# Kernel optimization log

Measured on AMD Instinct MI355X. Metric: run time of the kernel, lower is better.

## Reference

```python
import jax, jax.numpy as jnp
import numpy as np

N = 100000      # hits
K = 256         # max truth objects per event
C = 2           # n_ccoords
NCLS = 6        # n_classes
Q_MIN = 0.5
S_B = 1.0
ENERGY_DEN_OFFSET = 1.0
PAYLOAD_BETA_CLIP = 0.1
USE_AVG_CC = 0.0
BETA_CLIP = 1.0 - 1e-5


def _divide_no_nan(num, den):
    return jnp.where(den == 0.0, 0.0, num / jnp.where(den == 0.0, 1.0, den))


def setup_inputs() -> dict:
    key = jax.random.key(0)
    ks = jax.random.split(key, 12)
    pred_beta = jax.random.uniform(ks[0], (N, 1), minval=0.01, maxval=0.99)
    pred_ccoords = jax.random.normal(ks[1], (N, C))
    pred_energy = jax.random.uniform(ks[2], (N, 1), minval=0.0, maxval=100.0)
    pred_pos = 50.0 * jax.random.normal(ks[3], (N, 2))
    pred_time = jax.random.normal(ks[4], (N, 1))
    pred_id = jax.random.normal(ks[5], (N, NCLS))
    t_energy = jax.random.uniform(ks[6], (N, 1), minval=0.1, maxval=100.0)
    t_pos = 50.0 * jax.random.normal(ks[7], (N, 2))
    t_time = jax.random.normal(ks[8], (N, 1))
    t_pid = jax.random.randint(ks[9], (N, 1), 1, NCLS + 1).astype(jnp.float32)
    t_idx = jax.random.randint(ks[10], (N, 1), -1, K)  # -1 == noise
    rowsplits = jnp.array([0, N], dtype=jnp.int32)
    return dict(pred_beta=pred_beta, pred_ccoords=pred_ccoords,
                pred_energy=pred_energy, pred_pos=pred_pos,
                pred_time=pred_time, pred_id=pred_id,
                t_energy=t_energy, t_pos=t_pos, t_time=t_time, t_pid=t_pid,
                t_idx=t_idx, rowsplits=rowsplits)


def oc_loss(pred_beta, pred_ccoords, pred_energy, pred_pos, pred_time,
            pred_id, t_energy, t_pos, t_time, t_pid, t_idx):
    beta = jnp.clip(pred_beta[:, 0], 0.0, BETA_CLIP)          # [N]
    q = jnp.arctanh(beta) ** 2 + Q_MIN                        # [N] charge
    tidx = t_idx[:, 0]
    not_noise = tidx >= 0                                     # [N]
    tclip = jnp.where(not_noise, tidx, 0)

    # hit->object assignment matrix [N, K]
    M = jax.nn.one_hot(tclip, K, dtype=beta.dtype) * not_noise[:, None].astype(beta.dtype)
    counts = M.sum(axis=0)                                    # [K]
    obj_valid = counts > 0.0
    n_valid = jnp.maximum(obj_valid.sum().astype(beta.dtype), 1.0)

    # condensation point per object: highest-beta hit of that object
    score = jnp.where(M > 0.0, beta[:, None], -1.0)           # [N, K]
    alpha = jnp.argmax(score, axis=0)                         # [K]
    x_alpha = pred_ccoords[alpha]                             # [K, C]
    mean_cc = (M.T @ pred_ccoords) / jnp.maximum(counts, 1.0)[:, None]
    x_k = USE_AVG_CC * mean_cc + (1.0 - USE_AVG_CC) * x_alpha
    q_alpha = q[alpha]                                        # [K]
    beta_alpha = beta[alpha]

    # pairwise hit <-> condensation-point squared distances [N, K]
    diff = pred_ccoords[:, None, :] - x_k[None, :, :]
    distsq = jnp.sum(diff * diff, axis=-1)

    qq = q[:, None] * q_alpha[None, :]                        # [N, K]
    # attractive potential: own-object hits pulled toward condensation point
    v_att_k = (M * distsq * qq).sum(axis=0) / jnp.maximum(counts, 1.0)
    V_att = jnp.where(obj_valid, v_att_k, 0.0).sum() / n_valid
    # repulsive potential: all other hits pushed out of a unit ball
    hinge = jax.nn.relu(1.0 - jnp.sqrt(distsq + 1e-6))
    v_rep_k = ((1.0 - M) * hinge * qq).sum(axis=0) / jnp.maximum(N - counts, 1.0)
    V_rep = jnp.where(obj_valid, v_rep_k, 0.0).sum() / n_valid

    # beta terms: sharpen condensation points, suppress noise beta
    L_beta = jnp.where(obj_valid, 1.0 - beta_alpha, 0.0).sum() / n_valid
    n_noise = jnp.maximum((~not_noise).astype(beta.dtype).sum(), 1.0)
    L_noise = S_B * jnp.where(not_noise, 0.0, beta).sum() / n_noise

    # --- per-hit payload losses ---
    ew = jax.nn.relu(jnp.where(t_energy > 10.0,
                               1.0, (t_energy - 0.5) / 10.0 * 10.0 / 9.5))
    e_loss = _divide_no_nan((t_energy - pred_energy) ** 2,
                            t_energy + ENERGY_DEN_OFFSET)
    p_loss = jnp.sum((t_pos - pred_pos) ** 2, axis=-1, keepdims=True) / 100.0
    tm_loss = (t_time - pred_time) ** 2
    cls_loss = 1e-8 * jnp.mean(pred_id ** 2, axis=-1, keepdims=True)
    payload = jnp.concatenate([e_loss, p_loss, tm_loss, cls_loss], axis=-1) * ew  # [N,4]
    payload = jnp.where(pred_beta < PAYLOAD_BETA_CLIP, 0.0, payload)

    # beta-weighted average of payload over each truth object
    pw = beta * not_noise.astype(beta.dtype)                  # [N]
    num = M.T @ (payload * pw[:, None])                       # [K, 4]
    den = (M * pw[:, None]).sum(axis=0)                       # [K]
    per_obj = num / jnp.maximum(den, 1e-6)[:, None]
    L_payload = (jnp.where(obj_valid[:, None], per_obj, 0.0).sum(axis=0) / n_valid).sum()

    return V_att + V_rep + L_beta + L_noise + L_payload


def reference(pred_beta, pred_ccoords, pred_energy, pred_pos, pred_time,
              pred_id, t_energy, t_pos, t_time, t_pid, t_idx, rowsplits):
    return oc_loss(pred_beta, pred_ccoords, pred_energy, pred_pos, pred_time,
                   pred_id, t_energy, t_pos, t_time, t_pid, t_idx)
```

## Files before the change

### kernel.cpp

```cpp
#include <hip/hip_runtime.h>
#include <math.h>

#define KOBJ 256
#define B1   256
#define NW   4
#define WSTR 257
#define QMIN 0.5f
#define BETA_CLIP_C (1.0f - 1e-5f)

typedef unsigned long long u64;

__global__ __launch_bounds__(256) void partials(
    const float*  __restrict__ pred_beta,
    const float*  __restrict__ pred_energy,
    const float2* __restrict__ pred_pos,
    const float*  __restrict__ pred_time,
    const float2* __restrict__ pred_id2,
    const float*  __restrict__ t_energy,
    const float2* __restrict__ t_pos,
    const float*  __restrict__ t_time,
    const int*    __restrict__ t_idx,
    u64*    __restrict__ pk_part,
    float*  __restrict__ cnt_part,
    float*  __restrict__ den_part,
    float*  __restrict__ num_part,
    float*  __restrict__ noise_part,
    int n)
{
    __shared__ u64   spk[NW][WSTR];
    __shared__ float scnt[NW][WSTR], sden[NW][WSTR], snum[NW][WSTR];
    __shared__ float snoise[256];
    int t = threadIdx.x;
    int b = blockIdx.x;
    int w = t >> 6;
    for (int i = t; i < NW * WSTR; i += 256) {
        ((u64*)spk)[i] = 0;
        ((float*)scnt)[i] = 0.f;
        ((float*)sden)[i] = 0.f;
        ((float*)snum)[i] = 0.f;
    }
    __syncthreads();

    float noise = 0.0f;
    for (int i = b * 256 + t; i < n; i += B1 * 256) {
        int tid = t_idx[i];
        float braw = pred_beta[i];
        float beta = fminf(fmaxf(braw, 0.0f), BETA_CLIP_C);
        if (tid >= 0) {
            atomicAdd(&scnt[w][tid], 1.0f);
            u64 key = ((u64)__float_as_uint(beta) << 32) |
                      (u64)(0x7FFFFFFFu - (unsigned)i);
            atomicMax(&spk[w][tid], key);
            float te = t_energy[i];
            float ew = (te > 10.0f) ? 1.0f : fmaxf(0.0f, (te - 0.5f) / 9.5f);
            float de = te - pred_energy[i];
            float el = de * de / (te + 1.0f);
            float2 tp = t_pos[i];
            float2 pp = pred_pos[i];
            float dpx = tp.x - pp.x, dpy = tp.y - pp.y;
            float pl = (dpx * dpx + dpy * dpy) * 0.01f;
            float dt = t_time[i] - pred_time[i];
            float tl = dt * dt;
            float2 id0 = pred_id2[3 * i];
            float2 id1 = pred_id2[3 * i + 1];
            float2 id2 = pred_id2[3 * i + 2];
            float cs = id0.x * id0.x + id0.y * id0.y + id1.x * id1.x +
                       id1.y * id1.y + id2.x * id2.x + id2.y * id2.y;
            cs *= (1e-8f / 6.0f);
            float mask = (braw < 0.1f) ? 0.0f : 1.0f;
            float wgt = mask * ew * beta;
            atomicAdd(&sden[w][tid], beta);
            atomicAdd(&snum[w][tid], (el + pl + tl + cs) * wgt);
        } else {
            noise += beta;
        }
    }
    __syncthreads();
    u64 pk = spk[0][t];
    { u64 q = spk[1][t]; if (q > pk) pk = q; }
    { u64 q = spk[2][t]; if (q > pk) pk = q; }
    { u64 q = spk[3][t]; if (q > pk) pk = q; }
    float cnt = scnt[0][t] + scnt[1][t] + scnt[2][t] + scnt[3][t];
    float den = sden[0][t] + sden[1][t] + sden[2][t] + sden[3][t];
    float num = snum[0][t] + snum[1][t] + snum[2][t] + snum[3][t];
    int o = t * B1 + b;
    pk_part[o]  = pk;
    cnt_part[o] = cnt;
    den_part[o] = den;
    num_part[o] = num;
    snoise[t] = noise;
    __syncthreads();
    for (int s = 128; s > 0; s >>= 1) {
        if (t < s) snoise[t] += snoise[t + s];
        __syncthreads();
    }
    if (t == 0) noise_part[b] = snoise[0];
}

__global__ __launch_bounds__(256) void merge(
    const float2* __restrict__ pred_ccoords,
    const u64*    __restrict__ pk_part,
    const float*  __restrict__ cnt_part,
    const float*  __restrict__ den_part,
    const float*  __restrict__ num_part,
    float4* __restrict__ objA,
    float4* __restrict__ objB)
{
    __shared__ u64   spk[256];
    __shared__ float scnt[256], sden[256], snum[256];
    int k = blockIdx.x;
    int b = threadIdx.x;
    int o = k * B1 + b;
    u64 pk = pk_part[o];
    float cnt = cnt_part[o];
    float den = den_part[o];
    float nsum = num_part[o];
    spk[b] = pk; scnt[b] = cnt; sden[b] = den; snum[b] = nsum;
    __syncthreads();
    for (int s = 128; s > 0; s >>= 1) {
        if (b < s) {
            u64 p = spk[b + s]; if (p > spk[b]) spk[b] = p;
            scnt[b] += scnt[b + s];
            sden[b] += sden[b + s];
            snum[b] += snum[b + s];
        }
        __syncthreads();
    }
    if (b == 0) {
        float cs = scnt[0];
        bool valid = cs > 0.f;
        float xk = 0.f, yk = 0.f, qa = 0.f, lb = 0.f, pay = 0.f;
        if (valid) {
            u64 p = spk[0];
            unsigned a = 0x7FFFFFFFu - (unsigned)(p & 0xFFFFFFFFull);
            float ba = __uint_as_float((unsigned)(p >> 32));
            float2 cc = pred_ccoords[a];
            xk = cc.x; yk = cc.y;
            float at = atanhf(ba);
            qa = at * at + QMIN;
            lb = 1.0f - ba;
            pay = snum[0] / fmaxf(sden[0], 1e-6f);
        }
        objA[k] = make_float4(xk, yk, qa, cs);
        objB[k] = make_float4(pay, lb, valid ? 1.f : 0.f, 0.f);
    }
}

__global__ __launch_bounds__(256) void heavy(
    const float*  __restrict__ pred_beta,
    const float2* __restrict__ pred_ccoords,
    const int*    __restrict__ t_idx,
    const float4* __restrict__ objA,
    float* __restrict__ rep_part,
    float* __restrict__ att_part,
    int n, int hstr)
{
    __shared__ float4 pts[256];
    __shared__ float corrR[KOBJ], corrA[KOBJ];
    int t = threadIdx.x;
    corrR[t] = 0.f;
    corrA[t] = 0.f;
    int p = blockIdx.x * 256 + t;
    float4 pt;
    if (p < n) {
        float beta = fminf(fmaxf(pred_beta[p], 0.0f), BETA_CLIP_C);
        float at = atanhf(beta);
        float2 cc = pred_ccoords[p];
        pt = make_float4(cc.x, cc.y, at * at + QMIN, __int_as_float(t_idx[p]));
    } else {
        pt = make_float4(0.f, 0.f, 0.f, __int_as_float(-2));
    }
    pts[t] = pt;
    float4 oa = objA[t];
    float xk = oa.x, yk = oa.y;
    __syncthreads();

    int tid = __float_as_int(pt.w);
    if (tid >= 0) {
        float4 ok = objA[tid];
        float dx = pt.x - ok.x, dy = pt.y - ok.y;
        float d2 = fmaf(dy, dy, fmaf(dx, dx, 1e-6f));
        float r = __builtin_amdgcn_sqrtf(d2);
        float h = fmaxf(0.0f, 1.0f - r);
        atomicAdd(&corrA[tid], d2 * pt.z);
        atomicAdd(&corrR[tid], h * pt.z);
    }

    float rep = 0.f;
    #pragma unroll 8
    for (int j = 0; j < 256; ++j) {
        float4 s = pts[j];
        float dx = s.x - xk, dy = s.y - yk;
        float d2 = fmaf(dy, dy, fmaf(dx, dx, 1e-6f));
        float r = __builtin_amdgcn_sqrtf(d2);
        float h = fmaxf(0.0f, 1.0f - r);
        rep = fmaf(h, s.z, rep);
    }
    __syncthreads();
    int o = t * hstr + blockIdx.x;
    rep_part[o] = rep - corrR[t];
    att_part[o] = corrA[t];
}

__global__ __launch_bounds__(256) void final1(
    const float4* __restrict__ objA,
    const float4* __restrict__ objB,
    const float*  __restrict__ rep_part,
    const float*  __restrict__ att_part,
    float4* __restrict__ objC,
    int n, int nbh, int hstr)
{
    __shared__ float srep[256], satt[256];
    int k = blockIdx.x;
    int b = threadIdx.x;
    float rep = 0.f, att = 0.f;
    int o = k * hstr + b;
    if (b < nbh)        { rep += rep_part[o];        att += att_part[o]; }
    if (b + 256 < nbh)  { rep += rep_part[o + 256];  att += att_part[o + 256]; }
    srep[b] = rep; satt[b] = att;
    __syncthreads();
    for (int s = 128; s > 0; s >>= 1) {
        if (b < s) { srep[b] += srep[b + s]; satt[b] += satt[b + s]; }
        __syncthreads();
    }
    if (b == 0) {
        float4 a  = objA[k];
        float4 b4 = objB[k];
        float cnt = a.w, qa = a.z, valid = b4.z;
        float vatt = valid * satt[0] * qa / fmaxf(cnt, 1.0f);
        float vrep = valid * srep[0] * qa / fmaxf((float)n - cnt, 1.0f);
        objC[k] = make_float4(vatt + vrep + b4.y + b4.x, valid, cnt, 0.f);
    }
}

__global__ __launch_bounds__(256) void final2(
    const float4* __restrict__ objC,
    const float*  __restrict__ noise_part,
    float* __restrict__ out, int n)
{
    __shared__ float4 sred[256];
    int t = threadIdx.x;
    float4 c = objC[t];
    c.w = noise_part[t];
    sred[t] = c;
    __syncthreads();
    for (int s = 128; s > 0; s >>= 1) {
        if (t < s) {
            float4 x = sred[t], y = sred[t + s];
            sred[t] = make_float4(x.x + y.x, x.y + y.y, x.z + y.z, x.w + y.w);
        }
        __syncthreads();
    }
    if (t == 0) {
        float4 r = sred[0];
        float nv = fmaxf(r.y, 1.0f);
        float nnoise = fmaxf((float)n - r.z, 1.0f);
        out[0] = r.x / nv + r.w / nnoise;
    }
}

extern "C" void kernel_launch(void* const* d_in, const int* in_sizes, int n_in,
                              void* d_out, int out_size, void* d_ws, size_t ws_size,
                              hipStream_t stream) {
    const float*  pred_beta    = (const float*)d_in[0];
    const float2* pred_ccoords = (const float2*)d_in[1];
    const float*  pred_energy  = (const float*)d_in[2];
    const float2* pred_pos     = (const float2*)d_in[3];
    const float*  pred_time    = (const float*)d_in[4];
    const float2* pred_id2     = (const float2*)d_in[5];
    const float*  t_energy     = (const float*)d_in[6];
    const float2* t_pos        = (const float2*)d_in[7];
    const float*  t_time       = (const float*)d_in[8];
    const int*    t_idx        = (const int*)d_in[10];
    int n = in_sizes[0];
    int nbh = (n + 255) / 256;
    int hstr = (nbh + 8) & ~7;

    char* base = (char*)d_ws;
    size_t off = 0;
    u64*    pk_part    = (u64*)   (base + off); off += (size_t)KOBJ * B1 * 8;
    float*  cnt_part   = (float*) (base + off); off += (size_t)KOBJ * B1 * 4;
    float*  den_part   = (float*) (base + off); off += (size_t)KOBJ * B1 * 4;
    float*  num_part   = (float*) (base + off); off += (size_t)KOBJ * B1 * 4;
    float*  noise_part = (float*) (base + off); off += 256 * 4;
    float4* objA       = (float4*)(base + off); off += KOBJ * 16;
    float4* objB       = (float4*)(base + off); off += KOBJ * 16;
    float4* objC       = (float4*)(base + off); off += KOBJ * 16;
    float*  rep_part   = (float*) (base + off); off += (size_t)KOBJ * hstr * 4;
    float*  att_part   = (float*) (base + off); off += (size_t)KOBJ * hstr * 4;

    partials<<<B1, 256, 0, stream>>>(pred_beta, pred_energy, pred_pos, pred_time,
                                     pred_id2, t_energy, t_pos, t_time, t_idx,
                                     pk_part, cnt_part, den_part, num_part, noise_part, n);
    merge<<<KOBJ, 256, 0, stream>>>(pred_ccoords, pk_part, cnt_part, den_part, num_part,
                                    objA, objB);
    heavy<<<nbh, 256, 0, stream>>>(pred_beta, pred_ccoords, t_idx, objA,
                                   rep_part, att_part, n, hstr);
    final1<<<KOBJ, 256, 0, stream>>>(objA, objB, rep_part, att_part, objC, n, nbh, hstr);
    final2<<<1, 256, 0, stream>>>(objC, noise_part, (float*)d_out, n);
}
```

Measured before the change: 106.3 us.

## Fuse five kernels into one cooperative kernel with grid-wide syncs

Replaces the five separate launches with a single cooperative kernel that uses grid.sync() between the partials, merge, heavy, per-object finalize and final reduction phases. The partials phase now uses one block per 256 hits (nbh blocks) instead of 256 grid-striding blocks, so merge and final reductions loop over nbh partials. This is meant to remove launch gaps and inter-kernel overhead. In exchange it adds grid barrier costs and needs all ~391 blocks co-resident, which relies on the occupancy hint of 2 blocks per CU.

New measurement: 298.9 us. 181% more time.

```diff
diff --git a/kernel.cpp b/kernel.cpp
--- a/kernel.cpp
+++ b/kernel.cpp
@@ -1,8 +1,10 @@
 #include <hip/hip_runtime.h>
+#include <hip/hip_cooperative_groups.h>
 #include <math.h>
 
+namespace cg = cooperative_groups;
+
 #define KOBJ 256
-#define B1   256
 #define NW   4
 #define WSTR 257
 #define QMIN 0.5f
@@ -10,8 +12,11 @@
 
 typedef unsigned long long u64;
 
-__global__ __launch_bounds__(256) void partials(
+#define SM_BYTES 21600
+
+__global__ __launch_bounds__(256, 2) void fused(
     const float*  __restrict__ pred_beta,
+    const float2* __restrict__ pred_ccoords,
     const float*  __restrict__ pred_energy,
     const float2* __restrict__ pred_pos,
     const float*  __restrict__ pred_time,
@@ -25,237 +30,232 @@
     float*  __restrict__ den_part,
     float*  __restrict__ num_part,
     float*  __restrict__ noise_part,
-    int n)
+    float4* __restrict__ objA,
+    float4* __restrict__ objB,
+    float4* __restrict__ objC,
+    float*  __restrict__ rep_part,
+    float*  __restrict__ att_part,
+    float*  __restrict__ out,
+    int n, int nbh, int pstr)
 {
-    __shared__ u64   spk[NW][WSTR];
-    __shared__ float scnt[NW][WSTR], sden[NW][WSTR], snum[NW][WSTR];
-    __shared__ float snoise[256];
+    cg::grid_group grid = cg::this_grid();
+    __shared__ __align__(16) char smraw[SM_BYTES];
     int t = threadIdx.x;
     int b = blockIdx.x;
-    int w = t >> 6;
-    for (int i = t; i < NW * WSTR; i += 256) {
-        ((u64*)spk)[i] = 0;
-        ((float*)scnt)[i] = 0.f;
-        ((float*)sden)[i] = 0.f;
-        ((float*)snum)[i] = 0.f;
-    }
-    __syncthreads();
-
-    float noise = 0.0f;
-    for (int i = b * 256 + t; i < n; i += B1 * 256) {
-        int tid = t_idx[i];
-        float braw = pred_beta[i];
-        float beta = fminf(fmaxf(braw, 0.0f), BETA_CLIP_C);
+
+    {
+        u64   (*spk)[WSTR]  = reinterpret_cast<u64(*)[WSTR]>(smraw);
+        float (*scnt)[WSTR] = reinterpret_cast<float(*)[WSTR]>(smraw + 8224);
+        float (*sden)[WSTR] = reinterpret_cast<float(*)[WSTR]>(smraw + 12336);
+        float (*snum)[WSTR] = reinterpret_cast<float(*)[WSTR]>(smraw + 16448);
+        float  *snoise      = reinterpret_cast<float*>(smraw + 20560);
+        int w = t >> 6;
+        for (int i = t; i < NW * WSTR; i += 256) {
+            ((u64*)spk)[i] = 0;
+            ((float*)scnt)[i] = 0.f;
+            ((float*)sden)[i] = 0.f;
+            ((float*)snum)[i] = 0.f;
+        }
+        __syncthreads();
+
+        float noise = 0.0f;
+        int i = b * 256 + t;
+        if (i < n) {
+            int tid = t_idx[i];
+            float braw = pred_beta[i];
+            float beta = fminf(fmaxf(braw, 0.0f), BETA_CLIP_C);
+            if (tid >= 0) {
+                atomicAdd(&scnt[w][tid], 1.0f);
+                u64 key = ((u64)__float_as_uint(beta) << 32) |
+                          (u64)(0x7FFFFFFFu - (unsigned)i);
+                atomicMax(&spk[w][tid], key);
+                float te = t_energy[i];
+                float ew = (te > 10.0f) ? 1.0f : fmaxf(0.0f, (te - 0.5f) / 9.5f);
+                float de = te - pred_energy[i];
+                float el = de * de / (te + 1.0f);
+                float2 tp = t_pos[i];
+                float2 pp = pred_pos[i];
+                float dpx = tp.x - pp.x, dpy = tp.y - pp.y;
+                float pl = (dpx * dpx + dpy * dpy) * 0.01f;
+                float dt = t_time[i] - pred_time[i];
+                float tl = dt * dt;
+                float2 id0 = pred_id2[3 * i];
+                float2 id1 = pred_id2[3 * i + 1];
+                float2 id2 = pred_id2[3 * i + 2];
+                float cs = id0.x * id0.x + id0.y * id0.y + id1.x * id1.x +
+                           id1.y * id1.y + id2.x * id2.x + id2.y * id2.y;
+                cs *= (1e-8f / 6.0f);
+                float mask = (braw < 0.1f) ? 0.0f : 1.0f;
+                float wgt = mask * ew * beta;
+                atomicAdd(&sden[w][tid], beta);
+                atomicAdd(&snum[w][tid], (el + pl + tl + cs) * wgt);
+            } else {
+                noise = beta;
+            }
+        }
+        __syncthreads();
+        u64 pk = spk[0][t];
+        { u64 q = spk[1][t]; if (q > pk) pk = q; }
+        { u64 q = spk[2][t]; if (q > pk) pk = q; }
+        { u64 q = spk[3][t]; if (q > pk) pk = q; }
+        float cnt = scnt[0][t] + scnt[1][t] + scnt[2][t] + scnt[3][t];
+        float den = sden[0][t] + sden[1][t] + sden[2][t] + sden[3][t];
+        float num = snum[0][t] + snum[1][t] + snum[2][t] + snum[3][t];
+        int o = t * pstr + b;
+        pk_part[o]  = pk;
+        cnt_part[o] = cnt;
+        den_part[o] = den;
+        num_part[o] = num;
+        snoise[t] = noise;
+        __syncthreads();
+        for (int s = 128; s > 0; s >>= 1) {
+            if (t < s) snoise[t] += snoise[t + s];
+            __syncthreads();
+        }
+        if (t == 0) noise_part[b] = snoise[0];
+    }
+    grid.sync();
+
+    if (b < KOBJ) {
+        u64   *spk  = reinterpret_cast<u64*>(smraw);
+        float *scnt = reinterpret_cast<float*>(smraw + 2048);
+        float *sden = reinterpret_cast<float*>(smraw + 3072);
+        float *snum = reinterpret_cast<float*>(smraw + 4096);
+        u64 pk = 0;
+        float cnt = 0.f, den = 0.f, num = 0.f;
+        for (int j = t; j < nbh; j += 256) {
+            int o = b * pstr + j;
+            u64 q = pk_part[o]; if (q > pk) pk = q;
+            cnt += cnt_part[o]; den += den_part[o]; num += num_part[o];
+        }
+        spk[t] = pk; scnt[t] = cnt; sden[t] = den; snum[t] = num;
+        __syncthreads();
+        for (int s = 128; s > 0; s >>= 1) {
+            if (t < s) {
+                u64 p2 = spk[t + s]; if (p2 > spk[t]) spk[t] = p2;
+                scnt[t] += scnt[t + s];
+                sden[t] += sden[t + s];
+                snum[t] += snum[t + s];
+            }
+            __syncthreads();
+        }
+        if (t == 0) {
+            float cs = scnt[0];
+            bool valid = cs > 0.f;
+            float xk = 0.f, yk = 0.f, qa = 0.f, lb = 0.f, pay = 0.f;
+            if (valid) {
+                u64 p = spk[0];
+                unsigned a = 0x7FFFFFFFu - (unsigned)(p & 0xFFFFFFFFull);
+                float ba = __uint_as_float((unsigned)(p >> 32));
+                float2 cc = pred_ccoords[a];
+                xk = cc.x; yk = cc.y;
+                float at = atanhf(ba);
+                qa = at * at + QMIN;
+                lb = 1.0f - ba;
+                pay = snum[0] / fmaxf(sden[0], 1e-6f);
+            }
+            objA[b] = make_float4(xk, yk, qa, cs);
+            objB[b] = make_float4(pay, lb, valid ? 1.f : 0.f, 0.f);
+        }
+    }
+    grid.sync();
+
+    {
+        float4 *pts   = reinterpret_cast<float4*>(smraw);
+        float  *corrR = reinterpret_cast<float*>(smraw + 4096);
+        float  *corrA = reinterpret_cast<float*>(smraw + 5120);
+        corrR[t] = 0.f;
+        corrA[t] = 0.f;
+        int p = b * 256 + t;
+        float4 pt;
+        if (p < n) {
+            float beta = fminf(fmaxf(pred_beta[p], 0.0f), BETA_CLIP_C);
+            float at = atanhf(beta);
+            float2 cc = pred_ccoords[p];
+            pt = make_float4(cc.x, cc.y, at * at + QMIN, __int_as_float(t_idx[p]));
+        } else {
+            pt = make_float4(0.f, 0.f, 0.f, __int_as_float(-2));
+        }
+        pts[t] = pt;
+        float4 oa = objA[t];
+        float xk = oa.x, yk = oa.y;
+        __syncthreads();
+
+        int tid = __float_as_int(pt.w);
         if (tid >= 0) {
-            atomicAdd(&scnt[w][tid], 1.0f);
-            u64 key = ((u64)__float_as_uint(beta) << 32) |
-                      (u64)(0x7FFFFFFFu - (unsigned)i);
-            atomicMax(&spk[w][tid], key);
-            float te = t_energy[i];
-            float ew = (te > 10.0f) ? 1.0f : fmaxf(0.0f, (te - 0.5f) / 9.5f);
-            float de = te - pred_energy[i];
-            float el = de * de / (te + 1.0f);
-            float2 tp = t_pos[i];
-            float2 pp = pred_pos[i];
-            float dpx = tp.x - pp.x, dpy = tp.y - pp.y;
-            float pl = (dpx * dpx + dpy * dpy) * 0.01f;
-            float dt = t_time[i] - pred_time[i];
-            float tl = dt * dt;
-            float2 id0 = pred_id2[3 * i];
-            float2 id1 = pred_id2[3 * i + 1];
-            float2 id2 = pred_id2[3 * i + 2];
-            float cs = id0.x * id0.x + id0.y * id0.y + id1.x * id1.x +
-                       id1.y * id1.y + id2.x * id2.x + id2.y * id2.y;
-            cs *= (1e-8f / 6.0f);
-            float mask = (braw < 0.1f) ? 0.0f : 1.0f;
-            float wgt = mask * ew * beta;
-            atomicAdd(&sden[w][tid], beta);
-            atomicAdd(&snum[w][tid], (el + pl + tl + cs) * wgt);
-        } else {
-            noise += beta;
-        }
-    }
-    __syncthreads();
-    u64 pk = spk[0][t];
-    { u64 q = spk[1][t]; if (q > pk) pk = q; }
-    { u64 q = spk[2][t]; if (q > pk) pk = q; }
-    { u64 q = spk[3][t]; if (q > pk) pk = q; }
-    float cnt = scnt[0][t] + scnt[1][t] + scnt[2][t] + scnt[3][t];
-    float den = sden[0][t] + sden[1][t] + sden[2][t] + sden[3][t];
-    float num = snum[0][t] + snum[1][t] + snum[2][t] + snum[3][t];
-    int o = t * B1 + b;
-    pk_part[o]  = pk;
-    cnt_part[o] = cnt;
-    den_part[o] = den;
-    num_part[o] = num;
-    snoise[t] = noise;
-    __syncthreads();
-    for (int s = 128; s > 0; s >>= 1) {
-        if (t < s) snoise[t] += snoise[t + s];
-        __syncthreads();
-    }
-    if (t == 0) noise_part[b] = snoise[0];
-}
-
-__global__ __launch_bounds__(256) void merge(
-    const float2* __restrict__ pred_ccoords,
-    const u64*    __restrict__ pk_part,
-    const float*  __restrict__ cnt_part,
-    const float*  __restrict__ den_part,
-    const float*  __restrict__ num_part,
-    float4* __restrict__ objA,
-    float4* __restrict__ objB)
-{
-    __shared__ u64   spk[256];
-    __shared__ float scnt[256], sden[256], snum[256];
-    int k = blockIdx.x;
-    int b = threadIdx.x;
-    int o = k * B1 + b;
-    u64 pk = pk_part[o];
-    float cnt = cnt_part[o];
-    float den = den_part[o];
-    float nsum = num_part[o];
-    spk[b] = pk; scnt[b] = cnt; sden[b] = den; snum[b] = nsum;
-    __syncthreads();
-    for (int s = 128; s > 0; s >>= 1) {
-        if (b < s) {
-            u64 p = spk[b + s]; if (p > spk[b]) spk[b] = p;
-            scnt[b] += scnt[b + s];
-            sden[b] += sden[b + s];
-            snum[b] += snum[b + s];
-        }
-        __syncthreads();
-    }
+            float4 ok = objA[tid];
+            float dx = pt.x - ok.x, dy = pt.y - ok.y;
+            float d2 = fmaf(dy, dy, fmaf(dx, dx, 1e-6f));
+            float r = __builtin_amdgcn_sqrtf(d2);
+            float h = fmaxf(0.0f, 1.0f - r);
+            atomicAdd(&corrA[tid], d2 * pt.z);
+            atomicAdd(&corrR[tid], h * pt.z);
+        }
+
+        float rep = 0.f;
+        #pragma unroll 8
+        for (int j = 0; j < 256; ++j) {
+            float4 s = pts[j];
+            float dx = s.x - xk, dy = s.y - yk;
+            float d2 = fmaf(dy, dy, fmaf(dx, dx, 1e-6f));
+            float r = __builtin_amdgcn_sqrtf(d2);
+            float h = fmaxf(0.0f, 1.0f - r);
+            rep = fmaf(h, s.z, rep);
+        }
+        __syncthreads();
+        int o = t * pstr + b;
+        rep_part[o] = rep - corrR[t];
+        att_part[o] = corrA[t];
+    }
+    grid.sync();
+
+    if (b < KOBJ) {
+        float *srep = reinterpret_cast<float*>(smraw);
+        float *satt = reinterpret_cast<float*>(smraw + 1024);
+        float rep = 0.f, att = 0.f;
+        for (int j = t; j < nbh; j += 256) {
+            int o = b * pstr + j;
+            rep += rep_part[o];
+            att += att_part[o];
+        }
+        srep[t] = rep; satt[t] = att;
+        __syncthreads();
+        for (int s = 128; s > 0; s >>= 1) {
+            if (t < s) { srep[t] += srep[t + s]; satt[t] += satt[t + s]; }
+            __syncthreads();
+        }
+        if (t == 0) {
+            float4 a  = objA[b];
+            float4 b4 = objB[b];
+            float cnt = a.w, qa = a.z, valid = b4.z;
+            float vatt = valid * satt[0] * qa / fmaxf(cnt, 1.0f);
+            float vrep = valid * srep[0] * qa / fmaxf((float)n - cnt, 1.0f);
+            objC[b] = make_float4(vatt + vrep + b4.y + b4.x, valid, cnt, 0.f);
+        }
+    }
+    grid.sync();
+
     if (b == 0) {
-        float cs = scnt[0];
-        bool valid = cs > 0.f;
-        float xk = 0.f, yk = 0.f, qa = 0.f, lb = 0.f, pay = 0.f;
-        if (valid) {
-            u64 p = spk[0];
-            unsigned a = 0x7FFFFFFFu - (unsigned)(p & 0xFFFFFFFFull);
-            float ba = __uint_as_float((unsigned)(p >> 32));
-            float2 cc = pred_ccoords[a];
-            xk = cc.x; yk = cc.y;
-            float at = atanhf(ba);
-            qa = at * at + QMIN;
-            lb = 1.0f - ba;
-            pay = snum[0] / fmaxf(sden[0], 1e-6f);
-        }
-        objA[k] = make_float4(xk, yk, qa, cs);
-        objB[k] = make_float4(pay, lb, valid ? 1.f : 0.f, 0.f);
-    }
-}
-
-__global__ __launch_bounds__(256) void heavy(
-    const float*  __restrict__ pred_beta,
-    const float2* __restrict__ pred_ccoords,
-    const int*    __restrict__ t_idx,
-    const float4* __restrict__ objA,
-    float* __restrict__ rep_part,
-    float* __restrict__ att_part,
-    int n, int hstr)
-{
-    __shared__ float4 pts[256];
-    __shared__ float corrR[KOBJ], corrA[KOBJ];
-    int t = threadIdx.x;
-    corrR[t] = 0.f;
-    corrA[t] = 0.f;
-    int p = blockIdx.x * 256 + t;
-    float4 pt;
-    if (p < n) {
-        float beta = fminf(fmaxf(pred_beta[p], 0.0f), BETA_CLIP_C);
-        float at = atanhf(beta);
-        float2 cc = pred_ccoords[p];
-        pt = make_float4(cc.x, cc.y, at * at + QMIN, __int_as_float(t_idx[p]));
-    } else {
-        pt = make_float4(0.f, 0.f, 0.f, __int_as_float(-2));
-    }
-    pts[t] = pt;
-    float4 oa = objA[t];
-    float xk = oa.x, yk = oa.y;
-    __syncthreads();
-
-    int tid = __float_as_int(pt.w);
-    if (tid >= 0) {
-        float4 ok = objA[tid];
-        float dx = pt.x - ok.x, dy = pt.y - ok.y;
-        float d2 = fmaf(dy, dy, fmaf(dx, dx, 1e-6f));
-        float r = __builtin_amdgcn_sqrtf(d2);
-        float h = fmaxf(0.0f, 1.0f - r);
-        atomicAdd(&corrA[tid], d2 * pt.z);
-        atomicAdd(&corrR[tid], h * pt.z);
-    }
-
-    float rep = 0.f;
-    #pragma unroll 8
-    for (int j = 0; j < 256; ++j) {
-        float4 s = pts[j];
-        float dx = s.x - xk, dy = s.y - yk;
-        float d2 = fmaf(dy, dy, fmaf(dx, dx, 1e-6f));
-        float r = __builtin_amdgcn_sqrtf(d2);
-        float h = fmaxf(0.0f, 1.0f - r);
-        rep = fmaf(h, s.z, rep);
-    }
-    __syncthreads();
-    int o = t * hstr + blockIdx.x;
-    rep_part[o] = rep - corrR[t];
-    att_part[o] = corrA[t];
-}
-
-__global__ __launch_bounds__(256) void final1(
-    const float4* __restrict__ objA,
-    const float4* __restrict__ objB,
-    const float*  __restrict__ rep_part,
-    const float*  __restrict__ att_part,
-    float4* __restrict__ objC,
-    int n, int nbh, int hstr)
-{
-    __shared__ float srep[256], satt[256];
-    int k = blockIdx.x;
-    int b = threadIdx.x;
-    float rep = 0.f, att = 0.f;
-    int o = k * hstr + b;
-    if (b < nbh)        { rep += rep_part[o];        att += att_part[o]; }
-    if (b + 256 < nbh)  { rep += rep_part[o + 256];  att += att_part[o + 256]; }
-    srep[b] = rep; satt[b] = att;
-    __syncthreads();
-    for (int s = 128; s > 0; s >>= 1) {
-        if (b < s) { srep[b] += srep[b + s]; satt[b] += satt[b + s]; }
-        __syncthreads();
-    }
-    if (b == 0) {
-        float4 a  = objA[k];
-        float4 b4 = objB[k];
-        float cnt = a.w, qa = a.z, valid = b4.z;
-        float vatt = valid * satt[0] * qa / fmaxf(cnt, 1.0f);
-        float vrep = valid * srep[0] * qa / fmaxf((float)n - cnt, 1.0f);
-        objC[k] = make_float4(vatt + vrep + b4.y + b4.x, valid, cnt, 0.f);
-    }
-}
-
-__global__ __launch_bounds__(256) void final2(
-    const float4* __restrict__ objC,
-    const float*  __restrict__ noise_part,
-    float* __restrict__ out, int n)
-{
-    __shared__ float4 sred[256];
-    int t = threadIdx.x;
-    float4 c = objC[t];
-    c.w = noise_part[t];
-    sred[t] = c;
-    __syncthreads();
-    for (int s = 128; s > 0; s >>= 1) {
-        if (t < s) {
-            float4 x = sred[t], y = sred[t + s];
-            sred[t] = make_float4(x.x + y.x, x.y + y.y, x.z + y.z, x.w + y.w);
-        }
-        __syncthreads();
-    }
-    if (t == 0) {
-        float4 r = sred[0];
-        float nv = fmaxf(r.y, 1.0f);
-        float nnoise = fmaxf((float)n - r.z, 1.0f);
-        out[0] = r.x / nv + r.w / nnoise;
+        float4 *sred = reinterpret_cast<float4*>(smraw);
+        float4 c = objC[t];
+        float noi = 0.f;
+        for (int j = t; j < nbh; j += 256) noi += noise_part[j];
+        c.w = noi;
+        sred[t] = c;
+        __syncthreads();
+        for (int s = 128; s > 0; s >>= 1) {
+            if (t < s) {
+                float4 x = sred[t], y = sred[t + s];
+                sred[t] = make_float4(x.x + y.x, x.y + y.y, x.z + y.z, x.w + y.w);
+            }
+            __syncthreads();
+        }
+        if (t == 0) {
+            float4 r = sred[0];
+            float nv = fmaxf(r.y, 1.0f);
+            float nnoise = fmaxf((float)n - r.z, 1.0f);
+            out[0] = r.x / nv + r.w / nnoise;
+        }
     }
 }
 
@@ -274,28 +274,30 @@
     const int*    t_idx        = (const int*)d_in[10];
     int n = in_sizes[0];
     int nbh = (n + 255) / 256;
-    int hstr = (nbh + 8) & ~7;
+    int pstr = (nbh + 8) & ~7;
 
     char* base = (char*)d_ws;
     size_t off = 0;
-    u64*    pk_part    = (u64*)   (base + off); off += (size_t)KOBJ * B1 * 8;
-    float*  cnt_part   = (float*) (base + off); off += (size_t)KOBJ * B1 * 4;
-    float*  den_part   = (float*) (base + off); off += (size_t)KOBJ * B1 * 4;
-    float*  num_part   = (float*) (base + off); off += (size_t)KOBJ * B1 * 4;
-    float*  noise_part = (float*) (base + off); off += 256 * 4;
+    u64*    pk_part    = (u64*)   (base + off); off += (size_t)KOBJ * pstr * 8;
+    float*  cnt_part   = (float*) (base + off); off += (size_t)KOBJ * pstr * 4;
+    float*  den_part   = (float*) (base + off); off += (size_t)KOBJ * pstr * 4;
+    float*  num_part   = (float*) (base + off); off += (size_t)KOBJ * pstr * 4;
+    float*  noise_part = (float*) (base + off); off += (size_t)((nbh + 15) & ~15) * 4;
     float4* objA       = (float4*)(base + off); off += KOBJ * 16;
     float4* objB       = (float4*)(base + off); off += KOBJ * 16;
     float4* objC       = (float4*)(base + off); off += KOBJ * 16;
-    float*  rep_part   = (float*) (base + off); off += (size_t)KOBJ * hstr * 4;
-    float*  att_part   = (float*) (base + off); off += (size_t)KOBJ * hstr * 4;
-
-    partials<<<B1, 256, 0, stream>>>(pred_beta, pred_energy, pred_pos, pred_time,
-                                     pred_id2, t_energy, t_pos, t_time, t_idx,
-                                     pk_part, cnt_part, den_part, num_part, noise_part, n);
-    merge<<<KOBJ, 256, 0, stream>>>(pred_ccoords, pk_part, cnt_part, den_part, num_part,
-                                    objA, objB);
-    heavy<<<nbh, 256, 0, stream>>>(pred_beta, pred_ccoords, t_idx, objA,
-                                   rep_part, att_part, n, hstr);
-    final1<<<KOBJ, 256, 0, stream>>>(objA, objB, rep_part, att_part, objC, n, nbh, hstr);
-    final2<<<1, 256, 0, stream>>>(objC, noise_part, (float*)d_out, n);
+    float*  rep_part   = (float*) (base + off); off += (size_t)KOBJ * pstr * 4;
+    float*  att_part   = (float*) (base + off); off += (size_t)KOBJ * pstr * 4;
+    float*  outp       = (float*)d_out;
+
+    void* args[] = {
+        (void*)&pred_beta, (void*)&pred_ccoords, (void*)&pred_energy, (void*)&pred_pos,
+        (void*)&pred_time, (void*)&pred_id2, (void*)&t_energy, (void*)&t_pos,
+        (void*)&t_time, (void*)&t_idx,
+        (void*)&pk_part, (void*)&cnt_part, (void*)&den_part, (void*)&num_part,
+        (void*)&noise_part, (void*)&objA, (void*)&objB, (void*)&objC,
+        (void*)&rep_part, (void*)&att_part, (void*)&outp,
+        (void*)&n, (void*)&nbh, (void*)&pstr
+    };
+    hipLaunchCooperativeKernel((const void*)fused, dim3(nbh), dim3(256), args, 0, stream);
 }
```
